# Optimization experiments

Measured on AMD Instinct MI355X. Metric: run time of the kernel, lower is better.

## Reference

```python
import jax, jax.numpy as jnp
import numpy as np

B, H, S, D = 2, 8, 4096, 64
TEMPERATURE = 8.0


def setup_inputs() -> dict:
    key = jax.random.key(0)
    kq, kk, kv, km = jax.random.split(key, 4)
    q = jax.random.normal(kq, (B, H, S, D), dtype=jnp.float32)
    k = jax.random.normal(kk, (B, H, S, D), dtype=jnp.float32)
    v = jax.random.normal(kv, (B, H, S, D), dtype=jnp.float32)
    mask = jax.random.randint(km, (1, 1, S, S), 0, 2, dtype=jnp.int32)
    return {"q": q, "k": k, "v": v, "mask": mask}


def reference(q, k, v, mask):
    # scores = q @ k^T / temperature  -> [B,H,S,S]
    scores = jnp.einsum("bhqd,bhkd->bhqk", q, k) / TEMPERATURE
    # masked_fill(mask == 0, -inf)
    scores = jnp.where(mask == 0, -jnp.inf, scores)
    attn = jax.nn.softmax(scores, axis=-1)
    output = jnp.einsum("bhqk,bhkd->bhqd", attn, v)
    return (output, attn)
```

## Files before the change

kernel.cpp:

```cpp
#include <hip/hip_runtime.h>
#include <stdint.h>

typedef __attribute__((ext_vector_type(8))) short short8;
typedef __attribute__((ext_vector_type(4))) float float4v;

#define SEQ 4096
#define HD 64
#define QB 64
#define KT 64
#define HEADS 16
#define MWORDS (SEQ / 64)
#define TILE_BYTES 8192
#define QSCALE 0.18033688f

__device__ __forceinline__ ushort f2bf(float f) {
    union { float f; uint32_t u; } x; x.f = f;
    uint32_t u = x.u;
    return (ushort)((u + 0x7FFFu + ((u >> 16) & 1u)) >> 16);
}

__device__ __forceinline__ uint32_t cvt_pk_bf16(float lo, float hi) {
    uint32_t r;
    asm("v_cvt_pk_bf16_f32 %0, %1, %2" : "=v"(r) : "v"(lo), "v"(hi));
    return r;
}

__device__ __forceinline__ float exp2_hw(float x) { return __builtin_amdgcn_exp2f(x); }
__device__ __forceinline__ float log2_hw(float x) { return __builtin_amdgcn_logf(x); }

__device__ __forceinline__ void gload_lds16(const void* g, void* l) {
    __builtin_amdgcn_global_load_lds(
        (const __attribute__((address_space(1))) uint32_t*)g,
        (__attribute__((address_space(3))) uint32_t*)l, 16, 0, 0);
}

__global__ __launch_bounds__(256) void pack_mask_kernel(const int* __restrict__ mask,
                                                        unsigned long long* __restrict__ mb) {
    const int qrow = blockIdx.x;
    const int wave = threadIdx.x >> 6;
    const int lane = threadIdx.x & 63;
    const int* rp = mask + (size_t)qrow * SEQ;
    #pragma unroll
    for (int i = 0; i < 16; ++i) {
        const int widx = wave * 16 + i;
        const int mv = rp[widx * 64 + lane];
        unsigned long long b = __ballot(mv != 0);
        if (lane == 0) mb[(size_t)qrow * MWORDS + widx] = b;
    }
}

__global__ __launch_bounds__(256) void prep_kv_kernel(const float* __restrict__ kg,
                                                      const float* __restrict__ vg,
                                                      char* __restrict__ ktiles,
                                                      char* __restrict__ vtiles) {
    __shared__ __align__(16) float Tl[64][68];
    const int bid = blockIdx.x;
    const int tid = threadIdx.x;
    const float* Kg = kg + (size_t)bid * KT * HD;
    const float* Vg = vg + (size_t)bid * KT * HD;
    char* Kt = ktiles + (size_t)bid * TILE_BYTES;
    char* Vt = vtiles + (size_t)bid * TILE_BYTES;

    {
        const int r = tid >> 2, c0 = (tid & 3) * 16;
        #pragma unroll
        for (int j = 0; j < 4; ++j)
            *(float4v*)&Tl[r][c0 + j * 4] = *(const float4v*)(Kg + r * HD + c0 + j * 4);
    }
    __syncthreads();
    #pragma unroll
    for (int cc = 0; cc < 2; ++cc) {
        const int c = tid + cc * 256;
        const int t = c >> 7, h = (c >> 6) & 1, g = (c >> 4) & 3, li = c & 15;
        const int row = 32 * (t >> 1) + 8 * (li >> 2) + 4 * (t & 1) + (li & 3);
        const float* src = &Tl[row][h * 32 + g * 8];
        short8 w;
        #pragma unroll
        for (int e = 0; e < 8; ++e) w[e] = (short)f2bf(src[e]);
        *(short8*)(Kt + c * 16) = w;
    }
    __syncthreads();
    {
        const int r = tid >> 2, c0 = (tid & 3) * 16;
        #pragma unroll
        for (int j = 0; j < 4; ++j)
            *(float4v*)&Tl[r][c0 + j * 4] = *(const float4v*)(Vg + r * HD + c0 + j * 4);
    }
    __syncthreads();
    #pragma unroll
    for (int cc = 0; cc < 2; ++cc) {
        const int c = tid + cc * 256;
        const int dt = c >> 7, h = (c >> 6) & 1, g = (c >> 4) & 3, li = c & 15;
        short8 w;
        #pragma unroll
        for (int e = 0; e < 8; ++e) w[e] = (short)f2bf(Tl[h * 32 + g * 8 + e][dt * 16 + li]);
        *(short8*)(Vt + c * 16) = w;
    }
}

#define STAGE_K(KTI, DST) do {                                                     \
    const char* _s = Ktile + (size_t)(KTI) * TILE_BYTES + wave * 2048 + lane * 16; \
    char* _d = (char*)(DST) + wave * 2048;                                         \
    gload_lds16(_s, _d); gload_lds16(_s + 1024, _d + 1024);                        \
} while (0)

#define STAGE_V(KTI, DST) do {                                                     \
    const char* _s = Vtile + (size_t)(KTI) * TILE_BYTES + wave * 2048 + lane * 16; \
    char* _d = (char*)(DST) + wave * 2048;                                         \
    gload_lds16(_s, _d); gload_lds16(_s + 1024, _d + 1024);                        \
} while (0)

__global__ __launch_bounds__(256, 4) void attn_kernel(
    const float* __restrict__ qg, const unsigned long long* __restrict__ mb,
    const char* __restrict__ ktiles, const char* __restrict__ vtiles,
    float* __restrict__ outg, float* __restrict__ attng)
{
    __shared__ __align__(16) char Ks[2][TILE_BYTES];
    __shared__ __align__(16) char Vs[2][TILE_BYTES];

    const int tid  = threadIdx.x;
    const int wave = tid >> 6;
    const int lane = tid & 63;
    const int g    = lane >> 4;
    const int li   = lane & 15;

    const int bid = blockIdx.x;
    const int blk = (bid & 7) * 128 + (bid >> 3);
    const int bh  = blk >> 6;
    const int qb  = blk & 63;

    const size_t qkvBase = (size_t)bh * SEQ * HD;
    const float* Qg = qg + qkvBase + (size_t)qb * QB * HD;
    const char* Ktile = ktiles + (size_t)bh * (SEQ / KT) * TILE_BYTES;
    const char* Vtile = vtiles + (size_t)bh * (SEQ / KT) * TILE_BYTES;

    const int wq0 = wave * 16;
    short8 aq[2];
    #pragma unroll
    for (int h = 0; h < 2; ++h) {
        const float* src = Qg + (wq0 + li) * HD + h * 32 + g * 8;
        short8 t;
        #pragma unroll
        for (int e = 0; e < 8; ++e) t[e] = (short)f2bf(src[e] * QSCALE);
        aq[h] = t;
    }

    const int qrow = qb * QB + wq0 + li;
    const unsigned long long* mrow = mb + (size_t)qrow * MWORDS;

    STAGE_K(0, Ks[0]);
    __syncthreads();
    int cur = 0;
    float lsum = 0.f;
    for (int kt = 0; kt < SEQ / KT; ++kt) {
        if (kt < SEQ / KT - 1) STAGE_K(kt + 1, Ks[cur ^ 1]);
        const unsigned long long mw = mrow[kt];
        const uint32_t mlo = (uint32_t)mw >> (g * 8);
        const uint32_t mhi = (uint32_t)(mw >> 32) >> (g * 8);

        const char* Kb = Ks[cur] + lane * 16;
        short8 bk[4][2];
        #pragma unroll
        for (int t = 0; t < 4; ++t)
            #pragma unroll
            for (int h = 0; h < 2; ++h)
                bk[t][h] = *(const short8*)(Kb + (t * 2 + h) * 1024);

        float4v accs[4];
        #pragma unroll
        for (int t = 0; t < 4; ++t) accs[t] = (float4v){0.f, 0.f, 0.f, 0.f};
        #pragma unroll
        for (int t = 0; t < 4; ++t) {
            accs[t] = __builtin_amdgcn_mfma_f32_16x16x32_bf16(bk[t][0], aq[0], accs[t], 0, 0, 0);
            accs[t] = __builtin_amdgcn_mfma_f32_16x16x32_bf16(bk[t][1], aq[1], accs[t], 0, 0, 0);
        }
        const uint32_t nib[4] = { mlo & 0xFu, (mlo >> 4) & 0xFu, mhi & 0xFu, (mhi >> 4) & 0xFu };
        #pragma unroll
        for (int t = 0; t < 4; ++t) {
            #pragma unroll
            for (int r = 0; r < 4; ++r) {
                const float e = exp2_hw(accs[t][r]);
                lsum += ((nib[t] >> r) & 1u) ? e : 0.f;
            }
        }
        __syncthreads();
        cur ^= 1;
    }
    lsum += __shfl_xor(lsum, 16);
    lsum += __shfl_xor(lsum, 32);
    const float linv2 = -log2_hw(lsum);

    float* attnT = attng + (size_t)bh * SEQ * SEQ + (size_t)qrow * SEQ + g * 8;
    float4v acco[4];
    #pragma unroll
    for (int dt = 0; dt < 4; ++dt) acco[dt] = (float4v){0.f, 0.f, 0.f, 0.f};

    STAGE_K(0, Ks[0]);
    STAGE_V(0, Vs[0]);
    __syncthreads();
    cur = 0;
    for (int kt = 0; kt < SEQ / KT; ++kt) {
        if (kt < SEQ / KT - 1) { STAGE_K(kt + 1, Ks[cur ^ 1]); STAGE_V(kt + 1, Vs[cur ^ 1]); }
        const unsigned long long mw = mrow[kt];
        const uint32_t mlo = (uint32_t)mw >> (g * 8);
        const uint32_t mhi = (uint32_t)(mw >> 32) >> (g * 8);

        const char* Kb = Ks[cur] + lane * 16;
        short8 bk[4][2];
        #pragma unroll
        for (int t = 0; t < 4; ++t)
            #pragma unroll
            for (int h = 0; h < 2; ++h)
                bk[t][h] = *(const short8*)(Kb + (t * 2 + h) * 1024);

        float4v accs[4];
        #pragma unroll
        for (int t = 0; t < 4; ++t) accs[t] = (float4v){0.f, 0.f, 0.f, 0.f};
        #pragma unroll
        for (int t = 0; t < 4; ++t) {
            accs[t] = __builtin_amdgcn_mfma_f32_16x16x32_bf16(bk[t][0], aq[0], accs[t], 0, 0, 0);
            accs[t] = __builtin_amdgcn_mfma_f32_16x16x32_bf16(bk[t][1], aq[1], accs[t], 0, 0, 0);
        }

        const uint32_t nib[4] = { mlo & 0xFu, (mlo >> 4) & 0xFu, mhi & 0xFu, (mhi >> 4) & 0xFu };
        float4v pv[4];
        #pragma unroll
        for (int t = 0; t < 4; ++t) {
            #pragma unroll
            for (int r = 0; r < 4; ++r) {
                const float e = exp2_hw(accs[t][r] + linv2);
                pv[t][r] = ((nib[t] >> r) & 1u) ? e : 0.f;
            }
        }

        float* ap = attnT + kt * KT;
        *(float4v*)(ap)      = pv[0];
        *(float4v*)(ap + 4)  = pv[1];
        *(float4v*)(ap + 32) = pv[2];
        *(float4v*)(ap + 36) = pv[3];

        uint32_t pk[4][2];
        #pragma unroll
        for (int t = 0; t < 4; ++t) {
            pk[t][0] = cvt_pk_bf16(pv[t][0], pv[t][1]);
            pk[t][1] = cvt_pk_bf16(pv[t][2], pv[t][3]);
        }
        union { uint32_t u[4]; short8 s; } pa0, pa1;
        pa0.u[0] = pk[0][0]; pa0.u[1] = pk[0][1]; pa0.u[2] = pk[1][0]; pa0.u[3] = pk[1][1];
        pa1.u[0] = pk[2][0]; pa1.u[1] = pk[2][1]; pa1.u[2] = pk[3][0]; pa1.u[3] = pk[3][1];

        const char* Vb = Vs[cur] + lane * 16;
        #pragma unroll
        for (int dt = 0; dt < 4; ++dt) {
            short8 vb0 = *(const short8*)(Vb + (dt * 2 + 0) * 1024);
            short8 vb1 = *(const short8*)(Vb + (dt * 2 + 1) * 1024);
            acco[dt] = __builtin_amdgcn_mfma_f32_16x16x32_bf16(vb0, pa0.s, acco[dt], 0, 0, 0);
            acco[dt] = __builtin_amdgcn_mfma_f32_16x16x32_bf16(vb1, pa1.s, acco[dt], 0, 0, 0);
        }
        __syncthreads();
        cur ^= 1;
    }

    float* outW = outg + qkvBase + (size_t)qrow * HD + g * 4;
    #pragma unroll
    for (int dt = 0; dt < 4; ++dt) {
        *(float4v*)(outW + dt * 16) = acco[dt];
    }
}

extern "C" void kernel_launch(void* const* d_in, const int* in_sizes, int n_in,
                              void* d_out, int out_size, void* d_ws, size_t ws_size,
                              hipStream_t stream) {
    (void)in_sizes; (void)n_in; (void)out_size; (void)ws_size;
    const float* q = (const float*)d_in[0];
    const float* k = (const float*)d_in[1];
    const float* v = (const float*)d_in[2];
    const int* mask = (const int*)d_in[3];

    float* outp  = (float*)d_out;
    float* attnp = outp + (size_t)2 * 8 * SEQ * HD;

    char* ws = (char*)d_ws;
    unsigned long long* mb = (unsigned long long*)ws;
    char* ktiles = ws + (size_t)2 * 1024 * 1024;
    char* vtiles = ws + (size_t)10 * 1024 * 1024;

    pack_mask_kernel<<<SEQ, 256, 0, stream>>>(mask, mb);
    prep_kv_kernel<<<HEADS * (SEQ / KT), 256, 0, stream>>>(k, v, ktiles, vtiles);
    attn_kernel<<<HEADS * (SEQ / QB), 256, 0, stream>>>(q, mb, ktiles, vtiles, outp, attnp);
}
```

Baseline: 445.7 us.

## Load K/V fragments directly from global memory, dropping LDS double buffering

Removes the LDS staging buffers and the async global-to-LDS copies for K and V. Each wave now reads its MFMA fragments straight from global memory, relying on L1/L2 since all four waves read the same tile. This also drops the per-iteration block barriers and the LDS footprint, and lowers the occupancy hint from 4 to 3 blocks per CU to leave room for more registers. The risks are redundant global traffic (each wave loads the whole tile) and exposed load latency now that nothing prefetches the next tile.

```diff
diff --git a/kernel.cpp b/kernel.cpp
--- a/kernel.cpp
+++ b/kernel.cpp
@@ -27,12 +27,6 @@
 
 __device__ __forceinline__ float exp2_hw(float x) { return __builtin_amdgcn_exp2f(x); }
 __device__ __forceinline__ float log2_hw(float x) { return __builtin_amdgcn_logf(x); }
-
-__device__ __forceinline__ void gload_lds16(const void* g, void* l) {
-    __builtin_amdgcn_global_load_lds(
-        (const __attribute__((address_space(1))) uint32_t*)g,
-        (__attribute__((address_space(3))) uint32_t*)l, 16, 0, 0);
-}
 
 __global__ __launch_bounds__(256) void pack_mask_kernel(const int* __restrict__ mask,
                                                         unsigned long long* __restrict__ mb) {
@@ -98,26 +92,11 @@
     }
 }
 
-#define STAGE_K(KTI, DST) do {                                                     \
-    const char* _s = Ktile + (size_t)(KTI) * TILE_BYTES + wave * 2048 + lane * 16; \
-    char* _d = (char*)(DST) + wave * 2048;                                         \
-    gload_lds16(_s, _d); gload_lds16(_s + 1024, _d + 1024);                        \
-} while (0)
-
-#define STAGE_V(KTI, DST) do {                                                     \
-    const char* _s = Vtile + (size_t)(KTI) * TILE_BYTES + wave * 2048 + lane * 16; \
-    char* _d = (char*)(DST) + wave * 2048;                                         \
-    gload_lds16(_s, _d); gload_lds16(_s + 1024, _d + 1024);                        \
-} while (0)
-
-__global__ __launch_bounds__(256, 4) void attn_kernel(
+__global__ __launch_bounds__(256, 3) void attn_kernel(
     const float* __restrict__ qg, const unsigned long long* __restrict__ mb,
     const char* __restrict__ ktiles, const char* __restrict__ vtiles,
     float* __restrict__ outg, float* __restrict__ attng)
 {
-    __shared__ __align__(16) char Ks[2][TILE_BYTES];
-    __shared__ __align__(16) char Vs[2][TILE_BYTES];
-
     const int tid  = threadIdx.x;
     const int wave = tid >> 6;
     const int lane = tid & 63;
@@ -148,23 +127,18 @@
     const int qrow = qb * QB + wq0 + li;
     const unsigned long long* mrow = mb + (size_t)qrow * MWORDS;
 
-    STAGE_K(0, Ks[0]);
-    __syncthreads();
-    int cur = 0;
     float lsum = 0.f;
     for (int kt = 0; kt < SEQ / KT; ++kt) {
-        if (kt < SEQ / KT - 1) STAGE_K(kt + 1, Ks[cur ^ 1]);
+        const char* Kb = Ktile + (size_t)kt * TILE_BYTES + lane * 16;
+        short8 bk[4][2];
+        #pragma unroll
+        for (int t = 0; t < 4; ++t)
+            #pragma unroll
+            for (int h = 0; h < 2; ++h)
+                bk[t][h] = *(const short8*)(Kb + (t * 2 + h) * 1024);
         const unsigned long long mw = mrow[kt];
         const uint32_t mlo = (uint32_t)mw >> (g * 8);
         const uint32_t mhi = (uint32_t)(mw >> 32) >> (g * 8);
-
-        const char* Kb = Ks[cur] + lane * 16;
-        short8 bk[4][2];
-        #pragma unroll
-        for (int t = 0; t < 4; ++t)
-            #pragma unroll
-            for (int h = 0; h < 2; ++h)
-                bk[t][h] = *(const short8*)(Kb + (t * 2 + h) * 1024);
 
         float4v accs[4];
         #pragma unroll
@@ -183,8 +157,6 @@
                 lsum += ((nib[t] >> r) & 1u) ? e : 0.f;
             }
         }
-        __syncthreads();
-        cur ^= 1;
     }
     lsum += __shfl_xor(lsum, 16);
     lsum += __shfl_xor(lsum, 32);
@@ -195,23 +167,24 @@
     #pragma unroll
     for (int dt = 0; dt < 4; ++dt) acco[dt] = (float4v){0.f, 0.f, 0.f, 0.f};
 
-    STAGE_K(0, Ks[0]);
-    STAGE_V(0, Vs[0]);
-    __syncthreads();
-    cur = 0;
     for (int kt = 0; kt < SEQ / KT; ++kt) {
-        if (kt < SEQ / KT - 1) { STAGE_K(kt + 1, Ks[cur ^ 1]); STAGE_V(kt + 1, Vs[cur ^ 1]); }
+        const char* Kb = Ktile + (size_t)kt * TILE_BYTES + lane * 16;
+        const char* Vb = Vtile + (size_t)kt * TILE_BYTES + lane * 16;
+        short8 bk[4][2], vb[4][2];
+        #pragma unroll
+        for (int t = 0; t < 4; ++t)
+            #pragma unroll
+            for (int h = 0; h < 2; ++h)
+                bk[t][h] = *(const short8*)(Kb + (t * 2 + h) * 1024);
+        #pragma unroll
+        for (int t = 0; t < 4; ++t)
+            #pragma unroll
+            for (int h = 0; h < 2; ++h)
+                vb[t][h] = *(const short8*)(Vb + (t * 2 + h) * 1024);
+
         const unsigned long long mw = mrow[kt];
         const uint32_t mlo = (uint32_t)mw >> (g * 8);
         const uint32_t mhi = (uint32_t)(mw >> 32) >> (g * 8);
-
-        const char* Kb = Ks[cur] + lane * 16;
-        short8 bk[4][2];
-        #pragma unroll
-        for (int t = 0; t < 4; ++t)
-            #pragma unroll
-            for (int h = 0; h < 2; ++h)
-                bk[t][h] = *(const short8*)(Kb + (t * 2 + h) * 1024);
 
         float4v accs[4];
         #pragma unroll
@@ -249,16 +222,11 @@
         pa0.u[0] = pk[0][0]; pa0.u[1] = pk[0][1]; pa0.u[2] = pk[1][0]; pa0.u[3] = pk[1][1];
         pa1.u[0] = pk[2][0]; pa1.u[1] = pk[2][1]; pa1.u[2] = pk[3][0]; pa1.u[3] = pk[3][1];
 
-        const char* Vb = Vs[cur] + lane * 16;
         #pragma unroll
         for (int dt = 0; dt < 4; ++dt) {
-            short8 vb0 = *(const short8*)(Vb + (dt * 2 + 0) * 1024);
-            short8 vb1 = *(const short8*)(Vb + (dt * 2 + 1) * 1024);
-            acco[dt] = __builtin_amdgcn_mfma_f32_16x16x32_bf16(vb0, pa0.s, acco[dt], 0, 0, 0);
-            acco[dt] = __builtin_amdgcn_mfma_f32_16x16x32_bf16(vb1, pa1.s, acco[dt], 0, 0, 0);
-        }
-        __syncthreads();
-        cur ^= 1;
+            acco[dt] = __builtin_amdgcn_mfma_f32_16x16x32_bf16(vb[dt][0], pa0.s, acco[dt], 0, 0, 0);
+            acco[dt] = __builtin_amdgcn_mfma_f32_16x16x32_bf16(vb[dt][1], pa1.s, acco[dt], 0, 0, 0);
+        }
     }
 
     float* outW = outg + qkvBase + (size_t)qrow * HD + g * 4;
```

Result: slower. 631.9 us (+41.8%).

## Process two query sub-blocks per workgroup and defer attention-prob stores

Applied to the files above, without the earlier changes.

Each workgroup now handles 128 query rows, two 16-row groups per wave, so every staged K/V tile in LDS feeds twice as many MFMAs. This halves the K/V LDS staging and global traffic per query. The attention-probability stores are held in registers and written one iteration later so they overlap with the next tile's compute. The costs are higher register pressure (launch bounds lowered to 2 blocks), half as many workgroups, and lower occupancy.

```diff
diff --git a/kernel.cpp b/kernel.cpp
--- a/kernel.cpp
+++ b/kernel.cpp
@@ -6,9 +6,10 @@
 
 #define SEQ 4096
 #define HD 64
-#define QB 64
+#define QB 128
 #define KT 64
 #define HEADS 16
+#define NT (SEQ / KT)
 #define MWORDS (SEQ / 64)
 #define TILE_BYTES 8192
 #define QSCALE 0.18033688f
@@ -110,7 +111,7 @@
     gload_lds16(_s, _d); gload_lds16(_s + 1024, _d + 1024);                        \
 } while (0)
 
-__global__ __launch_bounds__(256, 4) void attn_kernel(
+__global__ __launch_bounds__(256, 2) void attn_kernel(
     const float* __restrict__ qg, const unsigned long long* __restrict__ mb,
     const char* __restrict__ ktiles, const char* __restrict__ vtiles,
     float* __restrict__ outg, float* __restrict__ attng)
@@ -125,38 +126,41 @@
     const int li   = lane & 15;
 
     const int bid = blockIdx.x;
-    const int blk = (bid & 7) * 128 + (bid >> 3);
-    const int bh  = blk >> 6;
-    const int qb  = blk & 63;
+    const int blk = (bid & 7) * 64 + (bid >> 3);
+    const int bh  = blk >> 5;
+    const int qb  = blk & 31;
 
     const size_t qkvBase = (size_t)bh * SEQ * HD;
     const float* Qg = qg + qkvBase + (size_t)qb * QB * HD;
-    const char* Ktile = ktiles + (size_t)bh * (SEQ / KT) * TILE_BYTES;
-    const char* Vtile = vtiles + (size_t)bh * (SEQ / KT) * TILE_BYTES;
+    const char* Ktile = ktiles + (size_t)bh * NT * TILE_BYTES;
+    const char* Vtile = vtiles + (size_t)bh * NT * TILE_BYTES;
 
     const int wq0 = wave * 16;
-    short8 aq[2];
-    #pragma unroll
-    for (int h = 0; h < 2; ++h) {
-        const float* src = Qg + (wq0 + li) * HD + h * 32 + g * 8;
-        short8 t;
-        #pragma unroll
-        for (int e = 0; e < 8; ++e) t[e] = (short)f2bf(src[e] * QSCALE);
-        aq[h] = t;
-    }
-
-    const int qrow = qb * QB + wq0 + li;
-    const unsigned long long* mrow = mb + (size_t)qrow * MWORDS;
+    short8 aq[2][2];
+    #pragma unroll
+    for (int u = 0; u < 2; ++u) {
+        #pragma unroll
+        for (int h = 0; h < 2; ++h) {
+            const float* src = Qg + (u * 64 + wq0 + li) * HD + h * 32 + g * 8;
+            short8 t;
+            #pragma unroll
+            for (int e = 0; e < 8; ++e) t[e] = (short)f2bf(src[e] * QSCALE);
+            aq[u][h] = t;
+        }
+    }
+
+    const int qrow0 = qb * QB + wq0 + li;
+    const int qrow1 = qrow0 + 64;
+    const unsigned long long* mrow0 = mb + (size_t)qrow0 * MWORDS;
+    const unsigned long long* mrow1 = mb + (size_t)qrow1 * MWORDS;
 
     STAGE_K(0, Ks[0]);
     __syncthreads();
     int cur = 0;
-    float lsum = 0.f;
-    for (int kt = 0; kt < SEQ / KT; ++kt) {
-        if (kt < SEQ / KT - 1) STAGE_K(kt + 1, Ks[cur ^ 1]);
-        const unsigned long long mw = mrow[kt];
-        const uint32_t mlo = (uint32_t)mw >> (g * 8);
-        const uint32_t mhi = (uint32_t)(mw >> 32) >> (g * 8);
+    float lsum[2] = {0.f, 0.f};
+    for (int kt = 0; kt < NT; ++kt) {
+        if (kt < NT - 1) STAGE_K(kt + 1, Ks[cur ^ 1]);
+        const unsigned long long mwv[2] = { mrow0[kt], mrow1[kt] };
 
         const char* Kb = Ks[cur] + lane * 16;
         short8 bk[4][2];
@@ -166,105 +170,150 @@
             for (int h = 0; h < 2; ++h)
                 bk[t][h] = *(const short8*)(Kb + (t * 2 + h) * 1024);
 
-        float4v accs[4];
-        #pragma unroll
-        for (int t = 0; t < 4; ++t) accs[t] = (float4v){0.f, 0.f, 0.f, 0.f};
-        #pragma unroll
-        for (int t = 0; t < 4; ++t) {
-            accs[t] = __builtin_amdgcn_mfma_f32_16x16x32_bf16(bk[t][0], aq[0], accs[t], 0, 0, 0);
-            accs[t] = __builtin_amdgcn_mfma_f32_16x16x32_bf16(bk[t][1], aq[1], accs[t], 0, 0, 0);
-        }
-        const uint32_t nib[4] = { mlo & 0xFu, (mlo >> 4) & 0xFu, mhi & 0xFu, (mhi >> 4) & 0xFu };
-        #pragma unroll
-        for (int t = 0; t < 4; ++t) {
-            #pragma unroll
-            for (int r = 0; r < 4; ++r) {
-                const float e = exp2_hw(accs[t][r]);
-                lsum += ((nib[t] >> r) & 1u) ? e : 0.f;
-            }
+        #pragma unroll
+        for (int u = 0; u < 2; ++u) {
+            const uint32_t mlo = (uint32_t)mwv[u] >> (g * 8);
+            const uint32_t mhi = (uint32_t)(mwv[u] >> 32) >> (g * 8);
+            const uint32_t nib[4] = { mlo & 0xFu, (mlo >> 4) & 0xFu, mhi & 0xFu, (mhi >> 4) & 0xFu };
+            float4v accs[4];
+            #pragma unroll
+            for (int t = 0; t < 4; ++t) accs[t] = (float4v){0.f, 0.f, 0.f, 0.f};
+            #pragma unroll
+            for (int t = 0; t < 4; ++t) {
+                accs[t] = __builtin_amdgcn_mfma_f32_16x16x32_bf16(bk[t][0], aq[u][0], accs[t], 0, 0, 0);
+                accs[t] = __builtin_amdgcn_mfma_f32_16x16x32_bf16(bk[t][1], aq[u][1], accs[t], 0, 0, 0);
+            }
+            float ls = 0.f;
+            #pragma unroll
+            for (int t = 0; t < 4; ++t)
+                #pragma unroll
+                for (int r = 0; r < 4; ++r) {
+                    const float e = exp2_hw(accs[t][r]);
+                    ls += ((nib[t] >> r) & 1u) ? e : 0.f;
+                }
+            lsum[u] += ls;
         }
         __syncthreads();
         cur ^= 1;
     }
-    lsum += __shfl_xor(lsum, 16);
-    lsum += __shfl_xor(lsum, 32);
-    const float linv2 = -log2_hw(lsum);
-
-    float* attnT = attng + (size_t)bh * SEQ * SEQ + (size_t)qrow * SEQ + g * 8;
-    float4v acco[4];
-    #pragma unroll
-    for (int dt = 0; dt < 4; ++dt) acco[dt] = (float4v){0.f, 0.f, 0.f, 0.f};
+    float linv2[2];
+    #pragma unroll
+    for (int u = 0; u < 2; ++u) {
+        float s = lsum[u];
+        s += __shfl_xor(s, 16);
+        s += __shfl_xor(s, 32);
+        linv2[u] = -log2_hw(s);
+    }
+
+    float* attnT0 = attng + (size_t)bh * SEQ * SEQ + (size_t)qrow0 * SEQ + g * 8;
+    float* attnT1 = attng + (size_t)bh * SEQ * SEQ + (size_t)qrow1 * SEQ + g * 8;
+    float4v acco[2][4];
+    #pragma unroll
+    for (int u = 0; u < 2; ++u)
+        #pragma unroll
+        for (int dt = 0; dt < 4; ++dt) acco[u][dt] = (float4v){0.f, 0.f, 0.f, 0.f};
+
+    float4v pvp0[4], pvp1[4];
 
     STAGE_K(0, Ks[0]);
     STAGE_V(0, Vs[0]);
     __syncthreads();
     cur = 0;
-    for (int kt = 0; kt < SEQ / KT; ++kt) {
-        if (kt < SEQ / KT - 1) { STAGE_K(kt + 1, Ks[cur ^ 1]); STAGE_V(kt + 1, Vs[cur ^ 1]); }
-        const unsigned long long mw = mrow[kt];
-        const uint32_t mlo = (uint32_t)mw >> (g * 8);
-        const uint32_t mhi = (uint32_t)(mw >> 32) >> (g * 8);
+    for (int kt = 0; kt < NT; ++kt) {
+        if (kt < NT - 1) { STAGE_K(kt + 1, Ks[cur ^ 1]); STAGE_V(kt + 1, Vs[cur ^ 1]); }
+        if (kt > 0) {
+            float* a0 = attnT0 + (kt - 1) * KT;
+            *(float4v*)(a0)      = pvp0[0];
+            *(float4v*)(a0 + 4)  = pvp0[1];
+            *(float4v*)(a0 + 32) = pvp0[2];
+            *(float4v*)(a0 + 36) = pvp0[3];
+            float* a1 = attnT1 + (kt - 1) * KT;
+            *(float4v*)(a1)      = pvp1[0];
+            *(float4v*)(a1 + 4)  = pvp1[1];
+            *(float4v*)(a1 + 32) = pvp1[2];
+            *(float4v*)(a1 + 36) = pvp1[3];
+        }
+        const unsigned long long mwv[2] = { mrow0[kt], mrow1[kt] };
 
         const char* Kb = Ks[cur] + lane * 16;
-        short8 bk[4][2];
+        const char* Vb = Vs[cur] + lane * 16;
+        short8 bk[4][2], vb[4][2];
         #pragma unroll
         for (int t = 0; t < 4; ++t)
             #pragma unroll
-            for (int h = 0; h < 2; ++h)
+            for (int h = 0; h < 2; ++h) {
                 bk[t][h] = *(const short8*)(Kb + (t * 2 + h) * 1024);
-
-        float4v accs[4];
-        #pragma unroll
-        for (int t = 0; t < 4; ++t) accs[t] = (float4v){0.f, 0.f, 0.f, 0.f};
-        #pragma unroll
-        for (int t = 0; t < 4; ++t) {
-            accs[t] = __builtin_amdgcn_mfma_f32_16x16x32_bf16(bk[t][0], aq[0], accs[t], 0, 0, 0);
-            accs[t] = __builtin_amdgcn_mfma_f32_16x16x32_bf16(bk[t][1], aq[1], accs[t], 0, 0, 0);
-        }
-
-        const uint32_t nib[4] = { mlo & 0xFu, (mlo >> 4) & 0xFu, mhi & 0xFu, (mhi >> 4) & 0xFu };
-        float4v pv[4];
-        #pragma unroll
-        for (int t = 0; t < 4; ++t) {
-            #pragma unroll
-            for (int r = 0; r < 4; ++r) {
-                const float e = exp2_hw(accs[t][r] + linv2);
-                pv[t][r] = ((nib[t] >> r) & 1u) ? e : 0.f;
-            }
-        }
-
-        float* ap = attnT + kt * KT;
-        *(float4v*)(ap)      = pv[0];
-        *(float4v*)(ap + 4)  = pv[1];
-        *(float4v*)(ap + 32) = pv[2];
-        *(float4v*)(ap + 36) = pv[3];
-
-        uint32_t pk[4][2];
-        #pragma unroll
-        for (int t = 0; t < 4; ++t) {
-            pk[t][0] = cvt_pk_bf16(pv[t][0], pv[t][1]);
-            pk[t][1] = cvt_pk_bf16(pv[t][2], pv[t][3]);
-        }
-        union { uint32_t u[4]; short8 s; } pa0, pa1;
-        pa0.u[0] = pk[0][0]; pa0.u[1] = pk[0][1]; pa0.u[2] = pk[1][0]; pa0.u[3] = pk[1][1];
-        pa1.u[0] = pk[2][0]; pa1.u[1] = pk[2][1]; pa1.u[2] = pk[3][0]; pa1.u[3] = pk[3][1];
-
-        const char* Vb = Vs[cur] + lane * 16;
-        #pragma unroll
-        for (int dt = 0; dt < 4; ++dt) {
-            short8 vb0 = *(const short8*)(Vb + (dt * 2 + 0) * 1024);
-            short8 vb1 = *(const short8*)(Vb + (dt * 2 + 1) * 1024);
-            acco[dt] = __builtin_amdgcn_mfma_f32_16x16x32_bf16(vb0, pa0.s, acco[dt], 0, 0, 0);
-            acco[dt] = __builtin_amdgcn_mfma_f32_16x16x32_bf16(vb1, pa1.s, acco[dt], 0, 0, 0);
+                vb[t][h] = *(const short8*)(Vb + (t * 2 + h) * 1024);
+            }
+
+        #pragma unroll
+        for (int u = 0; u < 2; ++u) {
+            const uint32_t mlo = (uint32_t)mwv[u] >> (g * 8);
+            const uint32_t mhi = (uint32_t)(mwv[u] >> 32) >> (g * 8);
+            const uint32_t nib[4] = { mlo & 0xFu, (mlo >> 4) & 0xFu, mhi & 0xFu, (mhi >> 4) & 0xFu };
+
+            float4v accs[4];
+            #pragma unroll
+            for (int t = 0; t < 4; ++t) accs[t] = (float4v){0.f, 0.f, 0.f, 0.f};
+            #pragma unroll
+            for (int t = 0; t < 4; ++t) {
+                accs[t] = __builtin_amdgcn_mfma_f32_16x16x32_bf16(bk[t][0], aq[u][0], accs[t], 0, 0, 0);
+                accs[t] = __builtin_amdgcn_mfma_f32_16x16x32_bf16(bk[t][1], aq[u][1], accs[t], 0, 0, 0);
+            }
+
+            float4v pv[4];
+            #pragma unroll
+            for (int t = 0; t < 4; ++t)
+                #pragma unroll
+                for (int r = 0; r < 4; ++r) {
+                    const float e = exp2_hw(accs[t][r] + linv2[u]);
+                    pv[t][r] = ((nib[t] >> r) & 1u) ? e : 0.f;
+                }
+
+            uint32_t pk[4][2];
+            #pragma unroll
+            for (int t = 0; t < 4; ++t) {
+                pk[t][0] = cvt_pk_bf16(pv[t][0], pv[t][1]);
+                pk[t][1] = cvt_pk_bf16(pv[t][2], pv[t][3]);
+            }
+            union { uint32_t w[4]; short8 s; } pa0, pa1;
+            pa0.w[0] = pk[0][0]; pa0.w[1] = pk[0][1]; pa0.w[2] = pk[1][0]; pa0.w[3] = pk[1][1];
+            pa1.w[0] = pk[2][0]; pa1.w[1] = pk[2][1]; pa1.w[2] = pk[3][0]; pa1.w[3] = pk[3][1];
+
+            #pragma unroll
+            for (int dt = 0; dt < 4; ++dt) {
+                acco[u][dt] = __builtin_amdgcn_mfma_f32_16x16x32_bf16(vb[dt][0], pa0.s, acco[u][dt], 0, 0, 0);
+                acco[u][dt] = __builtin_amdgcn_mfma_f32_16x16x32_bf16(vb[dt][1], pa1.s, acco[u][dt], 0, 0, 0);
+            }
+
+            #pragma unroll
+            for (int t = 0; t < 4; ++t) {
+                if (u == 0) pvp0[t] = pv[t]; else pvp1[t] = pv[t];
+            }
         }
         __syncthreads();
         cur ^= 1;
     }
-
-    float* outW = outg + qkvBase + (size_t)qrow * HD + g * 4;
-    #pragma unroll
-    for (int dt = 0; dt < 4; ++dt) {
-        *(float4v*)(outW + dt * 16) = acco[dt];
+    {
+        float* a0 = attnT0 + (NT - 1) * KT;
+        *(float4v*)(a0)      = pvp0[0];
+        *(float4v*)(a0 + 4)  = pvp0[1];
+        *(float4v*)(a0 + 32) = pvp0[2];
+        *(float4v*)(a0 + 36) = pvp0[3];
+        float* a1 = attnT1 + (NT - 1) * KT;
+        *(float4v*)(a1)      = pvp1[0];
+        *(float4v*)(a1 + 4)  = pvp1[1];
+        *(float4v*)(a1 + 32) = pvp1[2];
+        *(float4v*)(a1 + 36) = pvp1[3];
+    }
+
+    #pragma unroll
+    for (int u = 0; u < 2; ++u) {
+        float* outW = outg + qkvBase + (size_t)(u == 0 ? qrow0 : qrow1) * HD + g * 4;
+        #pragma unroll
+        for (int dt = 0; dt < 4; ++dt) {
+            *(float4v*)(outW + dt * 16) = acco[u][dt];
+        }
     }
 }
 
@@ -286,6 +335,6 @@
     char* vtiles = ws + (size_t)10 * 1024 * 1024;
 
     pack_mask_kernel<<<SEQ, 256, 0, stream>>>(mask, mb);
-    prep_kv_kernel<<<HEADS * (SEQ / KT), 256, 0, stream>>>(k, v, ktiles, vtiles);
+    prep_kv_kernel<<<HEADS * NT, 256, 0, stream>>>(k, v, ktiles, vtiles);
     attn_kernel<<<HEADS * (SEQ / QB), 256, 0, stream>>>(q, mb, ktiles, vtiles, outp, attnp);
 }
```

Result: slower. 512.3 us (+14.9%).

## Triple-buffer K in first pass, reorder second pass, add MFMA priority hints

Applied to the files above, without the earlier changes.

The first (row-sum) pass now uses a three-slot K ring with prefetch distance two, explicit vmcnt waits and raw barriers instead of full __syncthreads. The second pass hoists the V LDS reads next to the K reads, runs the PV MFMAs before the barrier, and moves the large attn-matrix global stores after the barrier so they overlap the next tile's work. s_setprio brackets the MFMA sections. The goal is to hide global-load latency and barrier stalls. The cost is more live registers for the V fragments and fragile manual waitcnt accounting.

```diff
diff --git a/kernel.cpp b/kernel.cpp
--- a/kernel.cpp
+++ b/kernel.cpp
@@ -9,6 +9,7 @@
 #define QB 64
 #define KT 64
 #define HEADS 16
+#define NT (SEQ / KT)
 #define MWORDS (SEQ / 64)
 #define TILE_BYTES 8192
 #define QSCALE 0.18033688f
@@ -115,8 +116,7 @@
     const char* __restrict__ ktiles, const char* __restrict__ vtiles,
     float* __restrict__ outg, float* __restrict__ attng)
 {
-    __shared__ __align__(16) char Ks[2][TILE_BYTES];
-    __shared__ __align__(16) char Vs[2][TILE_BYTES];
+    __shared__ __align__(16) char Lds[4][TILE_BYTES];
 
     const int tid  = threadIdx.x;
     const int wave = tid >> 6;
@@ -131,8 +131,8 @@
 
     const size_t qkvBase = (size_t)bh * SEQ * HD;
     const float* Qg = qg + qkvBase + (size_t)qb * QB * HD;
-    const char* Ktile = ktiles + (size_t)bh * (SEQ / KT) * TILE_BYTES;
-    const char* Vtile = vtiles + (size_t)bh * (SEQ / KT) * TILE_BYTES;
+    const char* Ktile = ktiles + (size_t)bh * NT * TILE_BYTES;
+    const char* Vtile = vtiles + (size_t)bh * NT * TILE_BYTES;
 
     const int wq0 = wave * 16;
     short8 aq[2];
@@ -148,17 +148,20 @@
     const int qrow = qb * QB + wq0 + li;
     const unsigned long long* mrow = mb + (size_t)qrow * MWORDS;
 
-    STAGE_K(0, Ks[0]);
-    __syncthreads();
-    int cur = 0;
+    STAGE_K(0, Lds[0]);
+    STAGE_K(1, Lds[1]);
+    asm volatile("s_waitcnt vmcnt(2)" ::: "memory");
+    __builtin_amdgcn_s_barrier();
+    asm volatile("" ::: "memory");
+
     float lsum = 0.f;
-    for (int kt = 0; kt < SEQ / KT; ++kt) {
-        if (kt < SEQ / KT - 1) STAGE_K(kt + 1, Ks[cur ^ 1]);
+    for (int kt = 0; kt < NT; ++kt) {
+        if (kt + 2 < NT) STAGE_K(kt + 2, Lds[(kt + 2) % 3]);
         const unsigned long long mw = mrow[kt];
         const uint32_t mlo = (uint32_t)mw >> (g * 8);
         const uint32_t mhi = (uint32_t)(mw >> 32) >> (g * 8);
 
-        const char* Kb = Ks[cur] + lane * 16;
+        const char* Kb = Lds[kt % 3] + lane * 16;
         short8 bk[4][2];
         #pragma unroll
         for (int t = 0; t < 4; ++t)
@@ -169,11 +172,13 @@
         float4v accs[4];
         #pragma unroll
         for (int t = 0; t < 4; ++t) accs[t] = (float4v){0.f, 0.f, 0.f, 0.f};
+        __builtin_amdgcn_s_setprio(1);
         #pragma unroll
         for (int t = 0; t < 4; ++t) {
             accs[t] = __builtin_amdgcn_mfma_f32_16x16x32_bf16(bk[t][0], aq[0], accs[t], 0, 0, 0);
             accs[t] = __builtin_amdgcn_mfma_f32_16x16x32_bf16(bk[t][1], aq[1], accs[t], 0, 0, 0);
         }
+        __builtin_amdgcn_s_setprio(0);
         const uint32_t nib[4] = { mlo & 0xFu, (mlo >> 4) & 0xFu, mhi & 0xFu, (mhi >> 4) & 0xFu };
         #pragma unroll
         for (int t = 0; t < 4; ++t) {
@@ -183,8 +188,12 @@
                 lsum += ((nib[t] >> r) & 1u) ? e : 0.f;
             }
         }
-        __syncthreads();
-        cur ^= 1;
+        if (kt < NT - 1) {
+            if (kt + 2 < NT) asm volatile("s_waitcnt vmcnt(3)" ::: "memory");
+            else             asm volatile("s_waitcnt vmcnt(1)" ::: "memory");
+            __builtin_amdgcn_s_barrier();
+            asm volatile("" ::: "memory");
+        }
     }
     lsum += __shfl_xor(lsum, 16);
     lsum += __shfl_xor(lsum, 32);
@@ -195,32 +204,38 @@
     #pragma unroll
     for (int dt = 0; dt < 4; ++dt) acco[dt] = (float4v){0.f, 0.f, 0.f, 0.f};
 
-    STAGE_K(0, Ks[0]);
-    STAGE_V(0, Vs[0]);
-    __syncthreads();
-    cur = 0;
-    for (int kt = 0; kt < SEQ / KT; ++kt) {
-        if (kt < SEQ / KT - 1) { STAGE_K(kt + 1, Ks[cur ^ 1]); STAGE_V(kt + 1, Vs[cur ^ 1]); }
+    __syncthreads();
+    STAGE_K(0, Lds[0]);
+    STAGE_V(0, Lds[2]);
+    __syncthreads();
+    for (int kt = 0; kt < NT; ++kt) {
+        const int b = kt & 1;
+        if (kt < NT - 1) { STAGE_K(kt + 1, Lds[b ^ 1]); STAGE_V(kt + 1, Lds[2 + (b ^ 1)]); }
         const unsigned long long mw = mrow[kt];
         const uint32_t mlo = (uint32_t)mw >> (g * 8);
         const uint32_t mhi = (uint32_t)(mw >> 32) >> (g * 8);
 
-        const char* Kb = Ks[cur] + lane * 16;
-        short8 bk[4][2];
+        const char* Kb = Lds[b] + lane * 16;
+        const char* Vb = Lds[2 + b] + lane * 16;
+        short8 bk[4][2], vb[4][2];
         #pragma unroll
         for (int t = 0; t < 4; ++t)
             #pragma unroll
-            for (int h = 0; h < 2; ++h)
+            for (int h = 0; h < 2; ++h) {
                 bk[t][h] = *(const short8*)(Kb + (t * 2 + h) * 1024);
+                vb[t][h] = *(const short8*)(Vb + (t * 2 + h) * 1024);
+            }
 
         float4v accs[4];
         #pragma unroll
         for (int t = 0; t < 4; ++t) accs[t] = (float4v){0.f, 0.f, 0.f, 0.f};
+        __builtin_amdgcn_s_setprio(1);
         #pragma unroll
         for (int t = 0; t < 4; ++t) {
             accs[t] = __builtin_amdgcn_mfma_f32_16x16x32_bf16(bk[t][0], aq[0], accs[t], 0, 0, 0);
             accs[t] = __builtin_amdgcn_mfma_f32_16x16x32_bf16(bk[t][1], aq[1], accs[t], 0, 0, 0);
         }
+        __builtin_amdgcn_s_setprio(0);
 
         const uint32_t nib[4] = { mlo & 0xFu, (mlo >> 4) & 0xFu, mhi & 0xFu, (mhi >> 4) & 0xFu };
         float4v pv[4];
@@ -233,32 +248,31 @@
             }
         }
 
+        uint32_t pk[4][2];
+        #pragma unroll
+        for (int t = 0; t < 4; ++t) {
+            pk[t][0] = cvt_pk_bf16(pv[t][0], pv[t][1]);
+            pk[t][1] = cvt_pk_bf16(pv[t][2], pv[t][3]);
+        }
+        union { uint32_t u[4]; short8 s; } pa0, pa1;
+        pa0.u[0] = pk[0][0]; pa0.u[1] = pk[0][1]; pa0.u[2] = pk[1][0]; pa0.u[3] = pk[1][1];
+        pa1.u[0] = pk[2][0]; pa1.u[1] = pk[2][1]; pa1.u[2] = pk[3][0]; pa1.u[3] = pk[3][1];
+
+        __builtin_amdgcn_s_setprio(1);
+        #pragma unroll
+        for (int dt = 0; dt < 4; ++dt) {
+            acco[dt] = __builtin_amdgcn_mfma_f32_16x16x32_bf16(vb[dt][0], pa0.s, acco[dt], 0, 0, 0);
+            acco[dt] = __builtin_amdgcn_mfma_f32_16x16x32_bf16(vb[dt][1], pa1.s, acco[dt], 0, 0, 0);
+        }
+        __builtin_amdgcn_s_setprio(0);
+
+        if (kt < NT - 1) __syncthreads();
+
         float* ap = attnT + kt * KT;
         *(float4v*)(ap)      = pv[0];
         *(float4v*)(ap + 4)  = pv[1];
         *(float4v*)(ap + 32) = pv[2];
         *(float4v*)(ap + 36) = pv[3];
-
-        uint32_t pk[4][2];
-        #pragma unroll
-        for (int t = 0; t < 4; ++t) {
-            pk[t][0] = cvt_pk_bf16(pv[t][0], pv[t][1]);
-            pk[t][1] = cvt_pk_bf16(pv[t][2], pv[t][3]);
-        }
-        union { uint32_t u[4]; short8 s; } pa0, pa1;
-        pa0.u[0] = pk[0][0]; pa0.u[1] = pk[0][1]; pa0.u[2] = pk[1][0]; pa0.u[3] = pk[1][1];
-        pa1.u[0] = pk[2][0]; pa1.u[1] = pk[2][1]; pa1.u[2] = pk[3][0]; pa1.u[3] = pk[3][1];
-
-        const char* Vb = Vs[cur] + lane * 16;
-        #pragma unroll
-        for (int dt = 0; dt < 4; ++dt) {
-            short8 vb0 = *(const short8*)(Vb + (dt * 2 + 0) * 1024);
-            short8 vb1 = *(const short8*)(Vb + (dt * 2 + 1) * 1024);
-            acco[dt] = __builtin_amdgcn_mfma_f32_16x16x32_bf16(vb0, pa0.s, acco[dt], 0, 0, 0);
-            acco[dt] = __builtin_amdgcn_mfma_f32_16x16x32_bf16(vb1, pa1.s, acco[dt], 0, 0, 0);
-        }
-        __syncthreads();
-        cur ^= 1;
     }
 
     float* outW = outg + qkvBase + (size_t)qrow * HD + g * 4;
@@ -286,6 +300,6 @@
     char* vtiles = ws + (size_t)10 * 1024 * 1024;
 
     pack_mask_kernel<<<SEQ, 256, 0, stream>>>(mask, mb);
-    prep_kv_kernel<<<HEADS * (SEQ / KT), 256, 0, stream>>>(k, v, ktiles, vtiles);
+    prep_kv_kernel<<<HEADS * NT, 256, 0, stream>>>(k, v, ktiles, vtiles);
     attn_kernel<<<HEADS * (SEQ / QB), 256, 0, stream>>>(q, mb, ktiles, vtiles, outp, attnp);
 }
```

Measured after the change: 414.2 us. 1.08x faster.
